# Performance work log

Hardware: AMD Instinct MI355X
Metric: run time of the kernel (lower is better)

Reference implementation:

```python
import jax, jax.numpy as jnp
import numpy as np
import math

B, SQ, SKV, H = 8, 1024, 1024, 1024
NH, HD = 16, 64  # num_attention_heads, attention_head_size


def setup_inputs() -> dict:
    key = jax.random.key(0)
    ks = jax.random.split(key, 6)
    s = 1.0 / math.sqrt(H)
    return {
        "hidden_states": jax.random.normal(ks[0], (B, SQ, H), jnp.float32),
        "keyvalue_states": jax.random.normal(ks[1], (B, SKV, H), jnp.float32),
        "attention_mask": jnp.zeros((B, 1, 1, SKV), jnp.float32),
        "Wq": jax.random.normal(ks[2], (H, H), jnp.float32) * s,
        "bq": jnp.zeros((H,), jnp.float32),
        "Wk": jax.random.normal(ks[3], (H, H), jnp.float32) * s,
        "bk": jnp.zeros((H,), jnp.float32),
        "Wv": jax.random.normal(ks[4], (H, H), jnp.float32) * s,
        "bv": jnp.zeros((H,), jnp.float32),
    }


def _split_heads(x):
    # [B, S, H] -> [B, NH, S, HD]
    b, s, _ = x.shape
    return x.reshape(b, s, NH, HD).transpose(0, 2, 1, 3)


def reference(hidden_states, keyvalue_states, attention_mask, Wq, bq, Wk, bk, Wv, bv):
    q = _split_heads(hidden_states @ Wq.T + bq)     # [B, NH, SQ, HD]
    k = _split_heads(keyvalue_states @ Wk.T + bk)   # [B, NH, SKV, HD]
    v = _split_heads(keyvalue_states @ Wv.T + bv)   # [B, NH, SKV, HD]
    scores = jnp.einsum("bhqd,bhkd->bhqk", q, k) / math.sqrt(HD)
    scores = scores + attention_mask                 # additive mask broadcast
    probs = jax.nn.softmax(scores, axis=-1)          # dropout = identity (eval)
    ctx = jnp.einsum("bhqk,bhkd->bhqd", probs, v)
    ctx = ctx.transpose(0, 2, 1, 3).reshape(hidden_states.shape[0], -1, NH * HD)
    return ctx
```

## Files before the change

kernel.cpp:

```cpp
#include <hip/hip_runtime.h>
#include <hip/hip_bf16.h>


typedef __attribute__((ext_vector_type(8))) short short8;
typedef __attribute__((ext_vector_type(4))) short short4v;
typedef __attribute__((ext_vector_type(4))) float f32x4;
typedef __attribute__((ext_vector_type(2))) float f32x2;
typedef __attribute__((ext_vector_type(16))) float f32x16;
typedef __attribute__((ext_vector_type(2))) unsigned uint2v;
typedef __attribute__((ext_vector_type(4))) int int4v;

#define AS1(p) ((const __attribute__((address_space(1))) void*)(p))
#define AS3(p) ((__attribute__((address_space(3))) void*)(p))

__device__ inline short f2bs(float x) {
    __hip_bfloat16 h = __float2bfloat16(x);
    return *reinterpret_cast<short*>(&h);
}

__global__ __launch_bounds__(256) void cvt_bf16(
    const float* __restrict__ s0, const float* __restrict__ s1,
    const float* __restrict__ s2, const float* __restrict__ s3,
    const float* __restrict__ s4,
    short* __restrict__ d0, short* __restrict__ d1,
    short* __restrict__ d2, short* __restrict__ d3, short* __restrict__ d4)
{
    const float* s; short* d; int n4;
    switch (blockIdx.y) {
        case 0: s = s0; d = d0; n4 = 2097152; break;
        case 1: s = s1; d = d1; n4 = 2097152; break;
        case 2: s = s2; d = d2; n4 = 262144;  break;
        case 3: s = s3; d = d3; n4 = 262144;  break;
        default: s = s4; d = d4; n4 = 262144; break;
    }
    for (int i = blockIdx.x * 256 + threadIdx.x; i < n4; i += gridDim.x * 256) {
        float4 v = ((const float4*)s)[i];
        short4v o;
        o.x = f2bs(v.x); o.y = f2bs(v.y); o.z = f2bs(v.z); o.w = f2bs(v.w);
        ((short4v*)d)[i] = o;
    }
}

__global__ __launch_bounds__(256) void qkv_gemm(
    const short* __restrict__ hsb, const short* __restrict__ kvb,
    const short* __restrict__ wqb, const short* __restrict__ wkb,
    const short* __restrict__ wvb,
    const float* __restrict__ bq, const float* __restrict__ bk,
    const float* __restrict__ bv,
    short* __restrict__ qo, short* __restrict__ ko, short* __restrict__ vo)
{
    const short* A; const short* W; const float* bias; short* dst;
    int z = blockIdx.z;
    if (z == 0)      { A = hsb; W = wqb; bias = bq; dst = qo; }
    else if (z == 1) { A = kvb; W = wkb; bias = bk; dst = ko; }
    else             { A = kvb; W = wvb; bias = bv; dst = vo; }

    __shared__ __align__(16) short As[128 * 64];
    __shared__ __align__(16) short Bs[128 * 64];

    const int t = threadIdx.x;
    const int lane = t & 63;
    const int wave = t >> 6;
    const int lane31 = lane & 31;
    const int hi = lane >> 5;
    const int wm = (wave & 1) * 64;
    const int wn = (wave >> 1) * 64;
    const int m0 = blockIdx.x * 128;
    const int n0 = blockIdx.y * 128;

    f32x16 acc[2][2] = {};

    for (int k0 = 0; k0 < 1024; k0 += 64) {
        #pragma unroll
        for (int i = 0; i < 4; ++i) {
            int c = i * 256 + t;
            int row = c >> 3;
            int gc = (c & 7) ^ (row & 7);
            __builtin_amdgcn_global_load_lds(
                AS1(&A[(size_t)(m0 + row) * 1024 + k0 + gc * 8]), AS3(&As[c * 8]), 16, 0, 0);
            __builtin_amdgcn_global_load_lds(
                AS1(&W[(size_t)(n0 + row) * 1024 + k0 + gc * 8]), AS3(&Bs[c * 8]), 16, 0, 0);
        }
        __syncthreads();

        #pragma unroll
        for (int kc = 0; kc < 4; ++kc) {
            short8 af[2], bf[2];
            #pragma unroll
            for (int mt = 0; mt < 2; ++mt) {
                int rr = wm + mt * 32 + lane31;
                af[mt] = *(short8*)&As[rr * 64 + ((kc * 2 + hi) ^ (rr & 7)) * 8];
            }
            #pragma unroll
            for (int nt = 0; nt < 2; ++nt) {
                int rn = wn + nt * 32 + lane31;
                bf[nt] = *(short8*)&Bs[rn * 64 + ((kc * 2 + hi) ^ (rn & 7)) * 8];
            }
            #pragma unroll
            for (int mt = 0; mt < 2; ++mt)
                #pragma unroll
                for (int nt = 0; nt < 2; ++nt)
                    acc[mt][nt] = __builtin_amdgcn_mfma_f32_32x32x16_bf16(
                        af[mt], bf[nt], acc[mt][nt], 0, 0, 0);
        }
        __syncthreads();
    }

    if (z != 2) {
        #pragma unroll
        for (int nt = 0; nt < 2; ++nt) {
            int col = n0 + wn + nt * 32 + lane31;
            float bb = bias[col];
            int h = col >> 6, d = col & 63;
            #pragma unroll
            for (int mt = 0; mt < 2; ++mt) {
                #pragma unroll
                for (int rg = 0; rg < 4; ++rg) {
                    int m = m0 + wm + mt * 32 + rg * 8 + hi * 4;
                    int b = m >> 10, s = m & 1023;
                    size_t base = (size_t)((b * 16 + h) * 1024 + s) * 64 + d;
                    #pragma unroll
                    for (int r = 0; r < 4; ++r)
                        dst[base + (size_t)r * 64] = f2bs(acc[mt][nt][rg * 4 + r] + bb);
                }
            }
        }
    } else {
        #pragma unroll
        for (int nt = 0; nt < 2; ++nt) {
            int col = n0 + wn + nt * 32 + lane31;
            float bb = bias[col];
            int h = col >> 6, d = col & 63;
            #pragma unroll
            for (int mt = 0; mt < 2; ++mt) {
                #pragma unroll
                for (int rg = 0; rg < 4; ++rg) {
                    int m = m0 + wm + mt * 32 + rg * 8 + hi * 4;
                    int b = m >> 10, s = m & 1023;
                    short4v pk;
                    pk.x = f2bs(acc[mt][nt][rg * 4 + 0] + bb);
                    pk.y = f2bs(acc[mt][nt][rg * 4 + 1] + bb);
                    pk.z = f2bs(acc[mt][nt][rg * 4 + 2] + bb);
                    pk.w = f2bs(acc[mt][nt][rg * 4 + 3] + bb);
                    *(short4v*)&dst[(size_t)((b * 16 + h) * 64 + d) * 1024 + s] = pk;
                }
            }
        }
    }
}

#define EXPC 0.18033688011112042f
#define LOG2E 1.4426950408889634f

__device__ inline uint2v half_swap(unsigned c, unsigned d, int hi) {
#if __has_builtin(__builtin_amdgcn_permlane32_swap)
    return __builtin_amdgcn_permlane32_swap(c, d, false, false);
#else
    unsigned send = hi ? c : d;
    unsigned recv = (unsigned)__shfl_xor((int)send, 32, 64);
    uint2v r;
    r.x = hi ? recv : c;
    r.y = hi ? d : recv;
    return r;
#endif
}

__device__ inline float fast_exp2(float x) {
#if __has_builtin(__builtin_amdgcn_exp2f)
    return __builtin_amdgcn_exp2f(x);
#else
    float r;
    asm("v_exp_f32 %0, %1" : "=v"(r) : "v"(x));
    return r;
#endif
}

__device__ inline unsigned cvt_pk_bf16(float a, float b) {
    unsigned r;
    asm("v_cvt_pk_bf16_f32 %0, %1, %2" : "=v"(r) : "v"(a), "v"(b));
    return r;
}

__global__ __launch_bounds__(256, 4) void attn(
    const short* __restrict__ q, const short* __restrict__ k,
    const short* __restrict__ vt, const float* __restrict__ mask,
    float* __restrict__ out)
{
    __shared__ __align__(16) short Ks[2][64 * 64];
    __shared__ __align__(16) short Vs[2][64 * 64];
    __shared__ __align__(16) float Ems[1024];

    const int t = threadIdx.x;
    const int lane = t & 63;
    const int wq = t >> 6;
    const int lane31 = lane & 31;
    const int hi = lane >> 5;

    const int id = blockIdx.x;
    const int bh = (id >> 6) * 8 + (id & 7);
    const int qt = (id >> 3) & 7;
    const int b = bh >> 4, h = bh & 15;

    const short* qbase = q + (size_t)(bh * 1024 + qt * 128) * 64;
    const short* kbase = k + (size_t)bh * 1024 * 64;
    const short* vbase = vt + (size_t)bh * 64 * 1024;

    {
        float4 mv = ((const float4*)(mask + b * 1024))[t];
        float4 o4;
        o4.x = mv.x * LOG2E; o4.y = mv.y * LOG2E;
        o4.z = mv.z * LOG2E; o4.w = mv.w * LOG2E;
        *(float4*)&Ems[t * 4] = o4;
    }

    short8 qf[4];
    #pragma unroll
    for (int kc = 0; kc < 4; ++kc)
        qf[kc] = *(const short8*)&qbase[(size_t)(wq * 32 + lane31) * 64 + kc * 16 + hi * 8];

    #pragma unroll
    for (int i = 0; i < 2; ++i) {
        int c = i * 256 + t;
        int row = c >> 3;
        int gc = (c & 7) ^ (row & 7);
        __builtin_amdgcn_global_load_lds(AS1(kbase + (size_t)row * 64 + gc * 8),
                                         AS3(&Ks[0][c * 8]), 16, 0, 0);
        __builtin_amdgcn_global_load_lds(AS1(vbase + (size_t)row * 1024 + gc * 8),
                                         AS3(&Vs[0][c * 8]), 16, 0, 0);
    }

    f32x16 o_acc[2] = {};
    f32x2 lacc = {0.f, 0.f};

    for (int kt = 0; kt < 16; ++kt) {
        __syncthreads();
        if (kt < 15) {
            int kv1 = (kt + 1) * 64;
            int nb = (kt + 1) & 1;
            #pragma unroll
            for (int i = 0; i < 2; ++i) {
                int c = i * 256 + t;
                int row = c >> 3;
                int gc = (c & 7) ^ (row & 7);
                __builtin_amdgcn_global_load_lds(
                    AS1(kbase + (size_t)(kv1 + row) * 64 + gc * 8),
                    AS3(&Ks[nb][c * 8]), 16, 0, 0);
                __builtin_amdgcn_global_load_lds(
                    AS1(vbase + (size_t)row * 1024 + kv1 + gc * 8),
                    AS3(&Vs[nb][c * 8]), 16, 0, 0);
            }
        }
        const short* ks_ = Ks[kt & 1];
        const short* vs_ = Vs[kt & 1];
        const int kv0 = kt * 64;

        f32x16 sacc[2] = {};
        #pragma unroll
        for (int kc = 0; kc < 4; ++kc) {
            #pragma unroll
            for (int mt = 0; mt < 2; ++mt) {
                int rr = mt * 32 + lane31;
                short8 ak = *(short8*)&ks_[rr * 64 + ((kc * 2 + hi) ^ (rr & 7)) * 8];
                sacc[mt] = __builtin_amdgcn_mfma_f32_32x32x16_bf16(ak, qf[kc], sacc[mt], 0, 0, 0);
            }
        }

        unsigned pk[2][4][2];
        #pragma unroll
        for (int mt = 0; mt < 2; ++mt) {
            #pragma unroll
            for (int rg = 0; rg < 4; ++rg) {
                int kvl = mt * 32 + rg * 8 + hi * 4;
                f32x4 mk = *(const f32x4*)&Ems[kv0 + kvl];
                f32x4 sv;
                sv.x = sacc[mt][rg * 4 + 0];
                sv.y = sacc[mt][rg * 4 + 1];
                sv.z = sacc[mt][rg * 4 + 2];
                sv.w = sacc[mt][rg * 4 + 3];
                f32x4 ev = sv * EXPC + mk;
                float p0 = fast_exp2(ev.x);
                float p1 = fast_exp2(ev.y);
                float p2 = fast_exp2(ev.z);
                float p3 = fast_exp2(ev.w);
                f32x2 pa; pa.x = p0; pa.y = p2;
                f32x2 pb; pb.x = p1; pb.y = p3;
                lacc += pa + pb;
                pk[mt][rg][0] = cvt_pk_bf16(p0, p1);
                pk[mt][rg][1] = cvt_pk_bf16(p2, p3);
            }
        }

        #pragma unroll
        for (int kc = 0; kc < 4; ++kc) {
            const int mt = kc >> 1, glo = (kc & 1) * 2;
            uint2v s0 = half_swap(pk[mt][glo][0], pk[mt][glo + 1][0], hi);
            uint2v s1 = half_swap(pk[mt][glo][1], pk[mt][glo + 1][1], hi);
            int4v fr; fr.x = (int)s0.x; fr.y = (int)s1.x; fr.z = (int)s0.y; fr.w = (int)s1.y;
            short8 ap = *(short8*)&fr;
            #pragma unroll
            for (int nt = 0; nt < 2; ++nt) {
                int rv = nt * 32 + lane31;
                short8 bv_ = *(short8*)&vs_[rv * 64 + ((kc * 2 + hi) ^ (rv & 7)) * 8];
                o_acc[nt] = __builtin_amdgcn_mfma_f32_32x32x16_bf16(ap, bv_, o_acc[nt], 0, 0, 0);
            }
        }
    }

    float l_sum = lacc.x + lacc.y;
    l_sum += __shfl_xor(l_sum, 32, 64);
    float invl = 1.f / l_sum;

    #pragma unroll
    for (int rg = 0; rg < 4; ++rg) {
        #pragma unroll
        for (int r = 0; r < 4; ++r) {
            int qrow_l = rg * 8 + hi * 4 + r;
            float lv = __shfl(invl, qrow_l, 64);
            int qrow = qt * 128 + wq * 32 + qrow_l;
            size_t base = (size_t)(b * 1024 + qrow) * 1024 + h * 64;
            #pragma unroll
            for (int nt = 0; nt < 2; ++nt)
                out[base + nt * 32 + lane31] = o_acc[nt][rg * 4 + r] * lv;
        }
    }
}

extern "C" void kernel_launch(void* const* d_in, const int* in_sizes, int n_in,
                              void* d_out, int out_size, void* d_ws, size_t ws_size,
                              hipStream_t stream) {
    const float* hs   = (const float*)d_in[0];
    const float* kvs  = (const float*)d_in[1];
    const float* mask = (const float*)d_in[2];
    const float* Wq   = (const float*)d_in[3];
    const float* bq   = (const float*)d_in[4];
    const float* Wk   = (const float*)d_in[5];
    const float* bk   = (const float*)d_in[6];
    const float* Wv   = (const float*)d_in[7];
    const float* bv   = (const float*)d_in[8];
    float* outp = (float*)d_out;

    const size_t big = (size_t)8 * 1024 * 1024;
    const size_t wsz = (size_t)1024 * 1024;
    short* q_ws  = (short*)d_ws;
    short* k_ws  = q_ws  + big;
    short* vt_ws = k_ws  + big;
    short* hsb   = vt_ws + big;
    short* kvb   = hsb   + big;
    short* wqb   = kvb   + big;
    short* wkb   = wqb   + wsz;
    short* wvb   = wkb   + wsz;

    cvt_bf16<<<dim3(1024, 5), 256, 0, stream>>>(hs, kvs, Wq, Wk, Wv,
                                                hsb, kvb, wqb, wkb, wvb);
    qkv_gemm<<<dim3(64, 8, 3), 256, 0, stream>>>(hsb, kvb, wqb, wkb, wvb,
                                                 bq, bk, bv, q_ws, k_ws, vt_ws);
    attn<<<dim3(1024), 256, 0, stream>>>(q_ws, k_ws, vt_ws, mask, outp);
}
```

Baseline: 230.7 us.

## Widen QKV GEMM tile to 256 columns, pack bf16 conversion, prioritize attention MFMAs

The QKV projection GEMM now computes a 128x256 output tile per block by loading two 128-row weight slabs, so each A tile in LDS is reused across twice as many columns. The grid halves along N, and launch bounds drop to 2 blocks per CU. The fp32-to-bf16 conversion kernel now handles 8 elements per thread with packed v_cvt_pk_bf16 instructions. The attention kernel wraps its MFMA sections in s_setprio to favor matrix issue. The larger GEMM tile raises register and LDS use and leaves fewer blocks (768), which may lower occupancy.

```diff
diff --git a/kernel.cpp b/kernel.cpp
--- a/kernel.cpp
+++ b/kernel.cpp
@@ -18,6 +18,12 @@
     return *reinterpret_cast<short*>(&h);
 }
 
+__device__ inline unsigned cvt_pk_bf16(float a, float b) {
+    unsigned r;
+    asm("v_cvt_pk_bf16_f32 %0, %1, %2" : "=v"(r) : "v"(a), "v"(b));
+    return r;
+}
+
 __global__ __launch_bounds__(256) void cvt_bf16(
     const float* __restrict__ s0, const float* __restrict__ s1,
     const float* __restrict__ s2, const float* __restrict__ s3,
@@ -25,23 +31,27 @@
     short* __restrict__ d0, short* __restrict__ d1,
     short* __restrict__ d2, short* __restrict__ d3, short* __restrict__ d4)
 {
-    const float* s; short* d; int n4;
+    const float* s; short* d; int n8;
     switch (blockIdx.y) {
-        case 0: s = s0; d = d0; n4 = 2097152; break;
-        case 1: s = s1; d = d1; n4 = 2097152; break;
-        case 2: s = s2; d = d2; n4 = 262144;  break;
-        case 3: s = s3; d = d3; n4 = 262144;  break;
-        default: s = s4; d = d4; n4 = 262144; break;
-    }
-    for (int i = blockIdx.x * 256 + threadIdx.x; i < n4; i += gridDim.x * 256) {
-        float4 v = ((const float4*)s)[i];
-        short4v o;
-        o.x = f2bs(v.x); o.y = f2bs(v.y); o.z = f2bs(v.z); o.w = f2bs(v.w);
-        ((short4v*)d)[i] = o;
-    }
-}
-
-__global__ __launch_bounds__(256) void qkv_gemm(
+        case 0: s = s0; d = d0; n8 = 1048576; break;
+        case 1: s = s1; d = d1; n8 = 1048576; break;
+        case 2: s = s2; d = d2; n8 = 131072;  break;
+        case 3: s = s3; d = d3; n8 = 131072;  break;
+        default: s = s4; d = d4; n8 = 131072; break;
+    }
+    for (int i = blockIdx.x * 256 + threadIdx.x; i < n8; i += gridDim.x * 256) {
+        float4 v0 = ((const float4*)s)[2 * i];
+        float4 v1 = ((const float4*)s)[2 * i + 1];
+        int4v o;
+        o.x = (int)cvt_pk_bf16(v0.x, v0.y);
+        o.y = (int)cvt_pk_bf16(v0.z, v0.w);
+        o.z = (int)cvt_pk_bf16(v1.x, v1.y);
+        o.w = (int)cvt_pk_bf16(v1.z, v1.w);
+        ((int4v*)d)[i] = o;
+    }
+}
+
+__global__ __launch_bounds__(256, 2) void qkv_gemm(
     const short* __restrict__ hsb, const short* __restrict__ kvb,
     const short* __restrict__ wqb, const short* __restrict__ wkb,
     const short* __restrict__ wvb,
@@ -50,13 +60,14 @@
     short* __restrict__ qo, short* __restrict__ ko, short* __restrict__ vo)
 {
     const short* A; const short* W; const float* bias; short* dst;
-    int z = blockIdx.z;
+    const int z = blockIdx.z;
     if (z == 0)      { A = hsb; W = wqb; bias = bq; dst = qo; }
     else if (z == 1) { A = kvb; W = wkb; bias = bk; dst = ko; }
     else             { A = kvb; W = wvb; bias = bv; dst = vo; }
 
     __shared__ __align__(16) short As[128 * 64];
-    __shared__ __align__(16) short Bs[128 * 64];
+    __shared__ __align__(16) short B1[128 * 64];
+    __shared__ __align__(16) short B2[128 * 64];
 
     const int t = threadIdx.x;
     const int lane = t & 63;
@@ -66,9 +77,9 @@
     const int wm = (wave & 1) * 64;
     const int wn = (wave >> 1) * 64;
     const int m0 = blockIdx.x * 128;
-    const int n0 = blockIdx.y * 128;
-
-    f32x16 acc[2][2] = {};
+    const int n0 = blockIdx.y * 256;
+
+    f32x16 acc[2][2][2] = {};
 
     for (int k0 = 0; k0 < 1024; k0 += 64) {
         #pragma unroll
@@ -79,13 +90,15 @@
             __builtin_amdgcn_global_load_lds(
                 AS1(&A[(size_t)(m0 + row) * 1024 + k0 + gc * 8]), AS3(&As[c * 8]), 16, 0, 0);
             __builtin_amdgcn_global_load_lds(
-                AS1(&W[(size_t)(n0 + row) * 1024 + k0 + gc * 8]), AS3(&Bs[c * 8]), 16, 0, 0);
+                AS1(&W[(size_t)(n0 + row) * 1024 + k0 + gc * 8]), AS3(&B1[c * 8]), 16, 0, 0);
+            __builtin_amdgcn_global_load_lds(
+                AS1(&W[(size_t)(n0 + 128 + row) * 1024 + k0 + gc * 8]), AS3(&B2[c * 8]), 16, 0, 0);
         }
         __syncthreads();
 
         #pragma unroll
         for (int kc = 0; kc < 4; ++kc) {
-            short8 af[2], bf[2];
+            short8 af[2], bf[2][2];
             #pragma unroll
             for (int mt = 0; mt < 2; ++mt) {
                 int rr = wm + mt * 32 + lane31;
@@ -94,55 +107,65 @@
             #pragma unroll
             for (int nt = 0; nt < 2; ++nt) {
                 int rn = wn + nt * 32 + lane31;
-                bf[nt] = *(short8*)&Bs[rn * 64 + ((kc * 2 + hi) ^ (rn & 7)) * 8];
-            }
-            #pragma unroll
-            for (int mt = 0; mt < 2; ++mt)
+                int off = rn * 64 + ((kc * 2 + hi) ^ (rn & 7)) * 8;
+                bf[0][nt] = *(short8*)&B1[off];
+                bf[1][nt] = *(short8*)&B2[off];
+            }
+            #pragma unroll
+            for (int nb = 0; nb < 2; ++nb)
                 #pragma unroll
-                for (int nt = 0; nt < 2; ++nt)
-                    acc[mt][nt] = __builtin_amdgcn_mfma_f32_32x32x16_bf16(
-                        af[mt], bf[nt], acc[mt][nt], 0, 0, 0);
+                for (int mt = 0; mt < 2; ++mt)
+                    #pragma unroll
+                    for (int nt = 0; nt < 2; ++nt)
+                        acc[nb][mt][nt] = __builtin_amdgcn_mfma_f32_32x32x16_bf16(
+                            af[mt], bf[nb][nt], acc[nb][mt][nt], 0, 0, 0);
         }
         __syncthreads();
     }
 
     if (z != 2) {
         #pragma unroll
-        for (int nt = 0; nt < 2; ++nt) {
-            int col = n0 + wn + nt * 32 + lane31;
-            float bb = bias[col];
-            int h = col >> 6, d = col & 63;
-            #pragma unroll
-            for (int mt = 0; mt < 2; ++mt) {
+        for (int nb = 0; nb < 2; ++nb) {
+            #pragma unroll
+            for (int nt = 0; nt < 2; ++nt) {
+                int col = n0 + nb * 128 + wn + nt * 32 + lane31;
+                float bb = bias[col];
+                int h = col >> 6, d = col & 63;
                 #pragma unroll
-                for (int rg = 0; rg < 4; ++rg) {
-                    int m = m0 + wm + mt * 32 + rg * 8 + hi * 4;
-                    int b = m >> 10, s = m & 1023;
-                    size_t base = (size_t)((b * 16 + h) * 1024 + s) * 64 + d;
+                for (int mt = 0; mt < 2; ++mt) {
                     #pragma unroll
-                    for (int r = 0; r < 4; ++r)
-                        dst[base + (size_t)r * 64] = f2bs(acc[mt][nt][rg * 4 + r] + bb);
+                    for (int rg = 0; rg < 4; ++rg) {
+                        int m = m0 + wm + mt * 32 + rg * 8 + hi * 4;
+                        int b = m >> 10, s = m & 1023;
+                        size_t base = (size_t)((b * 16 + h) * 1024 + s) * 64 + d;
+                        #pragma unroll
+                        for (int r = 0; r < 4; ++r)
+                            dst[base + (size_t)r * 64] = f2bs(acc[nb][mt][nt][rg * 4 + r] + bb);
+                    }
                 }
             }
         }
     } else {
         #pragma unroll
-        for (int nt = 0; nt < 2; ++nt) {
-            int col = n0 + wn + nt * 32 + lane31;
-            float bb = bias[col];
-            int h = col >> 6, d = col & 63;
-            #pragma unroll
-            for (int mt = 0; mt < 2; ++mt) {
+        for (int nb = 0; nb < 2; ++nb) {
+            #pragma unroll
+            for (int nt = 0; nt < 2; ++nt) {
+                int col = n0 + nb * 128 + wn + nt * 32 + lane31;
+                float bb = bias[col];
+                int h = col >> 6, d = col & 63;
                 #pragma unroll
-                for (int rg = 0; rg < 4; ++rg) {
-                    int m = m0 + wm + mt * 32 + rg * 8 + hi * 4;
-                    int b = m >> 10, s = m & 1023;
-                    short4v pk;
-                    pk.x = f2bs(acc[mt][nt][rg * 4 + 0] + bb);
-                    pk.y = f2bs(acc[mt][nt][rg * 4 + 1] + bb);
-                    pk.z = f2bs(acc[mt][nt][rg * 4 + 2] + bb);
-                    pk.w = f2bs(acc[mt][nt][rg * 4 + 3] + bb);
-                    *(short4v*)&dst[(size_t)((b * 16 + h) * 64 + d) * 1024 + s] = pk;
+                for (int mt = 0; mt < 2; ++mt) {
+                    #pragma unroll
+                    for (int rg = 0; rg < 4; ++rg) {
+                        int m = m0 + wm + mt * 32 + rg * 8 + hi * 4;
+                        int b = m >> 10, s = m & 1023;
+                        short4v pk;
+                        pk.x = f2bs(acc[nb][mt][nt][rg * 4 + 0] + bb);
+                        pk.y = f2bs(acc[nb][mt][nt][rg * 4 + 1] + bb);
+                        pk.z = f2bs(acc[nb][mt][nt][rg * 4 + 2] + bb);
+                        pk.w = f2bs(acc[nb][mt][nt][rg * 4 + 3] + bb);
+                        *(short4v*)&dst[(size_t)((b * 16 + h) * 64 + d) * 1024 + s] = pk;
+                    }
                 }
             }
         }
@@ -175,12 +198,6 @@
 #endif
 }
 
-__device__ inline unsigned cvt_pk_bf16(float a, float b) {
-    unsigned r;
-    asm("v_cvt_pk_bf16_f32 %0, %1, %2" : "=v"(r) : "v"(a), "v"(b));
-    return r;
-}
-
 __global__ __launch_bounds__(256, 4) void attn(
     const short* __restrict__ q, const short* __restrict__ k,
     const short* __restrict__ vt, const float* __restrict__ mask,
@@ -255,6 +272,7 @@
         const int kv0 = kt * 64;
 
         f32x16 sacc[2] = {};
+        __builtin_amdgcn_s_setprio(1);
         #pragma unroll
         for (int kc = 0; kc < 4; ++kc) {
             #pragma unroll
@@ -264,6 +282,7 @@
                 sacc[mt] = __builtin_amdgcn_mfma_f32_32x32x16_bf16(ak, qf[kc], sacc[mt], 0, 0, 0);
             }
         }
+        __builtin_amdgcn_s_setprio(0);
 
         unsigned pk[2][4][2];
         #pragma unroll
@@ -290,6 +309,7 @@
             }
         }
 
+        __builtin_amdgcn_s_setprio(1);
         #pragma unroll
         for (int kc = 0; kc < 4; ++kc) {
             const int mt = kc >> 1, glo = (kc & 1) * 2;
@@ -304,6 +324,7 @@
                 o_acc[nt] = __builtin_amdgcn_mfma_f32_32x32x16_bf16(ap, bv_, o_acc[nt], 0, 0, 0);
             }
         }
+        __builtin_amdgcn_s_setprio(0);
     }
 
     float l_sum = lacc.x + lacc.y;
@@ -352,7 +373,7 @@
 
     cvt_bf16<<<dim3(1024, 5), 256, 0, stream>>>(hs, kvs, Wq, Wk, Wv,
                                                 hsb, kvb, wqb, wkb, wvb);
-    qkv_gemm<<<dim3(64, 8, 3), 256, 0, stream>>>(hsb, kvb, wqb, wkb, wvb,
+    qkv_gemm<<<dim3(64, 4, 3), 256, 0, stream>>>(hsb, kvb, wqb, wkb, wvb,
                                                  bq, bk, bv, q_ws, k_ws, vt_ws);
     attn<<<dim3(1024), 256, 0, stream>>>(q_ws, k_ws, vt_ws, mask, outp);
 }
```

New measurement: 241.4 us. 1.05x slower.
